# Optimization experiments

Measured on AMD Instinct MI355X. Metric: run time of the kernel, lower is better.

The kernel has to match this reference:

```python
import jax, jax.numpy as jnp
import numpy as np

EPS = 1e-6
CHUNK = 256
N_HEADS = 16
GATE_NORM = 16.0


def rmsnorm(x, eps=EPS):
    # RMSNorm without affine; normalizes over the last axis (matches custom
    # RMSNorm applied pre-view over full dim for q/k/v and over head_dim for subln)
    return x * jax.lax.rsqrt(jnp.mean(x * x, axis=-1, keepdims=True) + eps)


def chunk_gate_retention(q, k, v, gt, chunk_size):
    """Chunked gated linear attention (RetNet/GLA-style).
    Recurrence: S_t = exp(g_t) * S_{t-1} + k_t^T v_t;  o_t = q_t @ S_t.
    q,k,v: (b,h,t,d); gt: (b,h,t) log-decay. Returns (o, last_state)."""
    b, h, t, d = q.shape
    c = chunk_size
    n = t // c
    scale = d ** -0.5
    q = q.reshape(b, h, n, c, d) * scale
    k = k.reshape(b, h, n, c, d)
    v = v.reshape(b, h, n, c, d)
    g = gt.reshape(b, h, n, c)
    bc = jnp.cumsum(g, axis=-1)            # cumulative log-decay within chunk (incl. own gate)
    B = bc[..., -1:]                        # total chunk log-decay (b,h,n,1)
    # ---- intra-chunk (causal, decayed) ----
    decay = jnp.exp(bc[..., :, None] - bc[..., None, :])  # (b,h,n,c,c), <=1 on/below diag
    mask = jnp.tril(jnp.ones((c, c), dtype=bool))
    A = jnp.einsum('bhnid,bhnjd->bhnij', q, k) * jnp.where(mask, decay, 0.0)
    o_intra = jnp.einsum('bhnij,bhnjd->bhnid', A, v)
    # ---- per-chunk kv summaries (decay from position j to chunk end) ----
    kd = k * jnp.exp(B - bc)[..., None]
    kv = jnp.einsum('bhncd,bhnce->bhnde', kd, v)          # (b,h,n,d,d)
    qd = q * jnp.exp(bc)[..., None]                        # state decay into position i
    # ---- inter-chunk recurrence over chunk index ----
    def step(S, inp):
        qd_n, kv_n, B_n = inp
        o_cross = jnp.einsum('bhcd,bhde->bhce', qd_n, S)
        S_new = jnp.exp(B_n)[..., None] * S + kv_n
        return S_new, o_cross
    S0 = jnp.zeros((b, h, d, d), dtype=q.dtype)
    inps = (jnp.moveaxis(qd, 2, 0), jnp.moveaxis(kv, 2, 0), jnp.moveaxis(B, 2, 0))
    S_last, o_cross = jax.lax.scan(step, S0, inps)
    o_cross = jnp.moveaxis(o_cross, 0, 2)                  # (b,h,n,c,d)
    o = (o_intra + o_cross).reshape(b, h, t, d)
    return o, S_last


def setup_inputs() -> dict:
    key = jax.random.key(0)
    ks = jax.random.split(key, 7)
    dim, nh = 1024, N_HEADS
    s = 0.03  # keep activations sane
    return {
        'x':   jax.random.normal(ks[0], (2, 8192, dim), dtype=jnp.float32),
        'Wq':  jax.random.normal(ks[1], (dim, dim), dtype=jnp.float32) * s,
        'Wk':  jax.random.normal(ks[2], (dim, dim), dtype=jnp.float32) * s,
        'Wv':  jax.random.normal(ks[3], (dim, dim), dtype=jnp.float32) * s,
        'Wg':  jax.random.normal(ks[4], (dim, dim), dtype=jnp.float32) * s,
        'Wgt': jax.random.normal(ks[5], (dim, nh), dtype=jnp.float32) * s,
        'Wo':  jax.random.normal(ks[6], (dim, dim), dtype=jnp.float32) * s,
    }


def reference(x, Wq, Wk, Wv, Wg, Wgt, Wo):
    b, t, dim = x.shape
    h = N_HEADS
    d = dim // h
    q = rmsnorm(x @ Wq)
    k = rmsnorm(x @ Wk)
    v = rmsnorm(x @ Wv)
    g = x @ Wg
    gt = jax.nn.log_sigmoid(x @ Wgt) / GATE_NORM   # (b,t,h)
    qr = q.reshape(b, t, h, d).transpose(0, 2, 1, 3)
    kr = k.reshape(b, t, h, d).transpose(0, 2, 1, 3)
    vr = v.reshape(b, t, h, d).transpose(0, 2, 1, 3)
    gtr = gt.transpose(0, 2, 1)                    # (b,h,t)
    o, _ = chunk_gate_retention(qr, kr, vr, gtr, CHUNK)
    o = rmsnorm(o)                                 # subln over head_dim
    o = o.transpose(0, 2, 1, 3).reshape(b, t, dim)
    o = jax.nn.silu(g) * o                         # swiglu(g, o)
    return o @ Wo
```

## Files before the change

### kernel.cpp

```cpp
#include <hip/hip_runtime.h>

#define T_SEQ 8192
#define NH 16
#define HD 64
#define DIM 1024
#define ROWS 16384
#define CHK 256
#define NCHK 32

typedef float f32x4 __attribute__((ext_vector_type(4)));
typedef __bf16 bf16x8 __attribute__((ext_vector_type(8)));
typedef short short8 __attribute__((ext_vector_type(8)));
typedef short short4v __attribute__((ext_vector_type(4)));
typedef unsigned short ushort_t;

__device__ __forceinline__ float bf2f(ushort_t u){ return __uint_as_float(((unsigned)u)<<16); }
__device__ __forceinline__ ushort_t f2bf(float f){
  unsigned u = __float_as_uint(f);
  u += 0x7FFFu + ((u>>16)&1u);
  return (ushort_t)(u>>16);
}
#define BFLO(u) __uint_as_float((u)<<16)
#define BFHI(u) __uint_as_float((u)&0xFFFF0000u)
#define MFMA16(a,b,c) __builtin_amdgcn_mfma_f32_16x16x32_bf16((a),(b),(c),0,0,0)

__global__ __launch_bounds__(256) void transpose_all(const float* __restrict__ Wq,
    const float* __restrict__ Wk, const float* __restrict__ Wv,
    const float* __restrict__ Wg, const float* __restrict__ Wo,
    ushort_t* __restrict__ wcat, ushort_t* __restrict__ wot){
  int z = blockIdx.z;
  const float* W = (z==0)?Wq:(z==1)?Wk:(z==2)?Wv:(z==3)?Wg:Wo;
  ushort_t* D = (z<4)? (wcat + (size_t)z*DIM*DIM) : wot;
  __shared__ float tile[64][65];
  int k0 = blockIdx.x*64, n0 = blockIdx.y*64;
  int tid = threadIdx.x;
  #pragma unroll
  for (int it=0; it<16; ++it){
    int idx = tid + it*256;
    int r = idx>>6, c = idx&63;
    tile[r][c] = W[(size_t)(k0+r)*DIM + n0+c];
  }
  __syncthreads();
  #pragma unroll
  for (int it=0; it<16; ++it){
    int idx = tid + it*256;
    int r = idx>>6, c = idx&63;
    D[(size_t)(n0+r)*DIM + k0+c] = f2bf(tile[c][r]);
  }
}

template<int OUT_BF16>
__global__ __launch_bounds__(256,2) void gemm_bt(const ushort_t* __restrict__ A,
    const ushort_t* __restrict__ Bt, void* __restrict__ Cv, int M, int N, int K,
    float* __restrict__ ssqp){
  __shared__ __align__(16) ushort_t As[128*64];
  __shared__ __align__(16) ushort_t Bs[128*64];
  int tid = threadIdx.x;
  int lane = tid & 63, wid = tid >> 6;
  int wr = wid >> 1, wc = wid & 1;
  int m0 = blockIdx.x * 128, n0 = blockIdx.y * 128;
  f32x4 acc[4][4] = {};
  int srow = tid >> 3;
  int sg = tid & 7;
  const int nkt = K >> 6;
  for (int kt = 0; kt < nkt; ++kt){
    short8 ra[4], rb[4];
    #pragma unroll
    for (int s = 0; s < 4; ++s){
      int row = s*32 + srow;
      int gl = sg ^ (row & 7);
      ra[s] = *(const short8*)&A[(size_t)(m0 + row)*K + kt*64 + gl*8];
      rb[s] = *(const short8*)&Bt[(size_t)(n0 + row)*K + kt*64 + gl*8];
    }
    __syncthreads();
    #pragma unroll
    for (int s = 0; s < 4; ++s){
      int row = s*32 + srow;
      *(short8*)&As[row*64 + sg*8] = ra[s];
      *(short8*)&Bs[row*64 + sg*8] = rb[s];
    }
    __syncthreads();
    #pragma unroll
    for (int kk = 0; kk < 2; ++kk){
      bf16x8 af[4], bfv[4];
      #pragma unroll
      for (int m = 0; m < 4; ++m){
        int row = wr*64 + m*16 + (lane & 15);
        int g = kk*4 + (lane >> 4);
        af[m] = *(const bf16x8*)&As[row*64 + ((g ^ (row & 7))<<3)];
      }
      #pragma unroll
      for (int n = 0; n < 4; ++n){
        int row = wc*64 + n*16 + (lane & 15);
        int g = kk*4 + (lane >> 4);
        bfv[n] = *(const bf16x8*)&Bs[row*64 + ((g ^ (row & 7))<<3)];
      }
      #pragma unroll
      for (int m = 0; m < 4; ++m)
        #pragma unroll
        for (int n = 0; n < 4; ++n)
          acc[m][n] = MFMA16(af[m], bfv[n], acc[m][n]);
    }
  }
  #pragma unroll
  for (int m = 0; m < 4; ++m){
    int row = m0 + wr*64 + m*16 + (lane>>4)*4;
    #pragma unroll
    for (int n = 0; n < 4; ++n){
      int col = n0 + wc*64 + n*16 + (lane & 15);
      #pragma unroll
      for (int r = 0; r < 4; ++r){
        float v = acc[m][n][r];
        if (OUT_BF16) ((ushort_t*)Cv)[(size_t)(row+r)*N + col] = f2bf(v);
        else          ((float*)Cv)[(size_t)(row+r)*N + col] = v;
      }
    }
  }
  if (OUT_BF16 && blockIdx.y < 24){
    int slot = blockIdx.y*2 + wc;
    #pragma unroll
    for (int m = 0; m < 4; ++m){
      #pragma unroll
      for (int r = 0; r < 4; ++r){
        float s = 0.f;
        #pragma unroll
        for (int n = 0; n < 4; ++n){ float xx = acc[m][n][r]; s += xx*xx; }
        s += __shfl_xor(s,1); s += __shfl_xor(s,2);
        s += __shfl_xor(s,4); s += __shfl_xor(s,8);
        if ((lane & 15) == 0){
          int row = m0 + wr*64 + m*16 + (lane>>4)*4 + r;
          ssqp[(size_t)slot*ROWS + row] = s;
        }
      }
    }
  }
}

__global__ __launch_bounds__(256) void rms_combine(const float* __restrict__ ssqp,
                                                   float* __restrict__ rmsb){
  int idx = blockIdx.x*256 + threadIdx.x;
  int mat = idx >> 14, row = idx & (ROWS-1);
  float s = 0.f;
  #pragma unroll
  for (int k=0;k<16;++k) s += ssqp[(size_t)(mat*16+k)*ROWS + row];
  rmsb[idx] = rsqrtf(s*(1.f/1024.f)+1e-6f);
}

__global__ __launch_bounds__(256) void gt_ker(const float* __restrict__ x,
    const float* __restrict__ Wgt, float* __restrict__ gtb, ushort_t* __restrict__ xbf){
  int row = blockIdx.x; int b = row>>13; int t = row & (T_SEQ-1);
  int tid = threadIdx.x; int lane = tid&63; int w = tid>>6;
  __shared__ float xs[1024];
  #pragma unroll
  for (int i=0;i<4;++i) xs[tid+256*i] = x[(size_t)row*DIM + tid+256*i];
  __syncthreads();
  short4v xb4;
  #pragma unroll
  for (int k2=0;k2<4;++k2) xb4[k2] = (short)f2bf(xs[tid*4+k2]);
  *(short4v*)&xbf[(size_t)row*DIM + tid*4] = xb4;
  float a0=0,a1=0,a2=0,a3=0;
  #pragma unroll
  for (int jj=0;jj<16;++jj){
    int j = lane + 64*jj;
    float xv = xs[j];
    const float* wp = &Wgt[(size_t)j*NH + w*4];
    a0 += xv*wp[0]; a1 += xv*wp[1]; a2 += xv*wp[2]; a3 += xv*wp[3];
  }
  #pragma unroll
  for (int off=32; off>=1; off>>=1){
    a0 += __shfl_xor(a0, off); a1 += __shfl_xor(a1, off);
    a2 += __shfl_xor(a2, off); a3 += __shfl_xor(a3, off);
  }
  if (lane==0){
    float za[4] = {a0,a1,a2,a3};
    #pragma unroll
    for (int i=0;i<4;++i){
      float z = za[i];
      float ls = fminf(z,0.f) - log1pf(__expf(-fabsf(z)));
      gtb[((size_t)(b*NH + w*4 + i))*T_SEQ + t] = ls * (1.f/16.f);
    }
  }
}

__global__ __launch_bounds__(256,2) void attn_p1(const ushort_t* __restrict__ qkvg,
    const float* __restrict__ gtb, const float* __restrict__ rmsb,
    float* __restrict__ Bb, float* __restrict__ kvb){
  __shared__ __align__(16) ushort_t sh2[32768];
  ushort_t* kdt = sh2;
  ushort_t* vt  = sh2 + 16384;
  float* tmp = (float*)sh2;
  int bid = blockIdx.x; int n = bid&31; int bh = bid>>5; int b = bh>>4; int h = bh&15;
  int t0 = n*CHK; int tid = threadIdx.x; int lane = tid&63; int w = tid>>6;
  float vscan = gtb[(size_t)bh*T_SEQ + t0 + tid];
  #pragma unroll
  for (int off=1; off<64; off<<=1){ float u = __shfl_up(vscan, off); if (lane>=off) vscan += u; }
  if (lane==63) tmp[w] = vscan;
  __syncthreads();
  float pre=0;
  #pragma unroll
  for (int i=0;i<4;++i) if (i<w) pre += tmp[i];
  float bc = vscan + pre;
  float Bn = tmp[0]+tmp[1]+tmp[2]+tmp[3];
  if (tid==0) Bb[bid] = Bn;
  __syncthreads();
  {
    int j = tid;
    int grow = b*T_SEQ + t0 + j;
    size_t rowb = (size_t)grow*4096;
    float fk = rmsb[ROWS + grow] * __expf(Bn - bc);
    float fv = rmsb[2*ROWS + grow];
    #pragma unroll
    for (int q8=0; q8<8; ++q8){
      short8 k8 = *(const short8*)&qkvg[rowb + 1024 + h*HD + q8*8];
      short8 v8 = *(const short8*)&qkvg[rowb + 2048 + h*HD + q8*8];
      #pragma unroll
      for (int kk=0; kk<8; ++kk){
        int d = q8*8 + kk;
        kdt[(d<<8) + (((j>>3)^(d&7))<<3) + (j&7)] = f2bf(bf2f((ushort_t)k8[kk])*fk);
        vt [(d<<8) + (((j>>3)^(d&7))<<3) + (j&7)] = f2bf(bf2f((ushort_t)v8[kk])*fv);
      }
    }
  }
  __syncthreads();
  f32x4 acc[4] = {};
  #pragma unroll
  for (int s=0; s<8; ++s){
    int d = w*16 + (lane&15);
    int jj = s*32 + (lane>>4)*8;
    bf16x8 ka = *(const bf16x8*)&kdt[(d<<8) + (((jj>>3)^(d&7))<<3)];
    #pragma unroll
    for (int et=0; et<4; ++et){
      int e = et*16 + (lane&15);
      bf16x8 vf = *(const bf16x8*)&vt[(e<<8) + (((jj>>3)^(e&7))<<3)];
      acc[et] = MFMA16(ka, vf, acc[et]);
    }
  }
  float* kvp = &kvb[(size_t)bid*4096];
  #pragma unroll
  for (int et=0; et<4; ++et)
    #pragma unroll
    for (int r=0; r<4; ++r)
      kvp[(et*16 + (lane&15))*64 + w*16 + (lane>>4)*4 + r] = acc[et][r];
}

__global__ __launch_bounds__(256) void scan_ker(const float* __restrict__ kvb,
    const float* __restrict__ Bb, ushort_t* __restrict__ Sb){
  int gidx = blockIdx.x*256 + threadIdx.x;
  int bh = gidx >> 12; int f = gidx & 4095;
  float S = 0.f;
  const float* kp = &kvb[(size_t)bh*NCHK*4096 + f];
  ushort_t* sp = &Sb[(size_t)bh*NCHK*4096 + f];
  for (int n=0;n<NCHK;++n){
    sp[(size_t)n*4096] = f2bf(S);
    S = __expf(Bb[bh*NCHK+n])*S + kp[(size_t)n*4096];
  }
}

__global__ __launch_bounds__(512,2) void attn_p3(const ushort_t* __restrict__ qkvg,
    const float* __restrict__ gtb, const float* __restrict__ rmsb,
    const ushort_t* __restrict__ Sb, ushort_t* __restrict__ oact){
  __shared__ __align__(16) ushort_t sh[(32768+16384+1024+32+2048)/2];
  ushort_t* vt = sh;
  ushort_t* ps = sh + 16384;
  float* bcs = (float*)(sh + 24576);
  float* tmp = (float*)(sh + 25088);
  float* rqs = (float*)(sh + 25104);
  float* rks = (float*)(sh + 25616);
  int bid = blockIdx.x; int n = bid&31; int bh = bid>>5; int b = bh>>4; int h = bh&15;
  int t0 = n*CHK; int tid = threadIdx.x; int lane = tid&63; int w = tid>>6;
  float vscan = 0.f;
  if (tid < 256){
    vscan = gtb[(size_t)bh*T_SEQ + t0 + tid];
    #pragma unroll
    for (int off=1; off<64; off<<=1){ float u = __shfl_up(vscan, off); if (lane>=off) vscan += u; }
    if (lane==63) tmp[w] = vscan;
  }
  __syncthreads();
  if (tid < 256){
    float pre=0;
    #pragma unroll
    for (int i=0;i<4;++i) if (i<w) pre += tmp[i];
    bcs[tid] = vscan + pre;
    int grow = b*T_SEQ + t0 + tid;
    rqs[tid] = rmsb[grow];
    rks[tid] = rmsb[ROWS + grow];
  }
  {
    int j = tid>>1, ehalf = tid&1;
    int grow = b*T_SEQ + t0 + j;
    size_t rowb = (size_t)grow*4096;
    float fv = rmsb[2*ROWS + grow];
    #pragma unroll
    for (int q8=0; q8<4; ++q8){
      short8 v8 = *(const short8*)&qkvg[rowb + 2048 + h*HD + ehalf*32 + q8*8];
      #pragma unroll
      for (int kk=0; kk<8; ++kk){
        int e = ehalf*32 + q8*8 + kk;
        vt[(e<<8) + (((j>>3)^(e&7))<<3) + (j&7)] = f2bf(bf2f((ushort_t)v8[kk])*fv);
      }
    }
  }
  __syncthreads();
  int wrow = w*32;
  size_t chunkbase = (size_t)b*T_SEQ + t0;
  bf16x8 qf[2][2];
  #pragma unroll
  for (int rt=0; rt<2; ++rt)
    #pragma unroll
    for (int s=0; s<2; ++s)
      qf[rt][s] = *(const bf16x8*)&qkvg[(chunkbase + wrow + rt*16 + (lane&15))*4096
                                        + h*HD + s*32 + (lane>>4)*8];
  f32x4 o_[2][4] = {};
  #pragma unroll
  for (int s=0; s<2; ++s)
    #pragma unroll
    for (int et=0; et<4; ++et){
      bf16x8 stf = *(const bf16x8*)&Sb[(size_t)bid*4096 + (et*16 + (lane&15))*64
                                       + s*32 + (lane>>4)*8];
      #pragma unroll
      for (int rt=0; rt<2; ++rt)
        o_[rt][et] = MFMA16(qf[rt][s], stf, o_[rt][et]);
    }
  #pragma unroll
  for (int rt=0; rt<2; ++rt)
    #pragma unroll
    for (int rr=0; rr<4; ++rr){
      int ri = wrow + rt*16 + (lane>>4)*4 + rr;
      float fs = 0.125f*__expf(bcs[ri])*rqs[ri];
      #pragma unroll
      for (int et=0; et<4; ++et) o_[rt][et][rr] *= fs;
    }
  for (int hb=0; hb<=w; ++hb){
    int jb = hb>>1, ch = hb&1;
    int jbase = jb*64 + ch*32;
    float mb = bcs[jb*64];
    float r8[2][4];
    #pragma unroll
    for (int rt=0; rt<2; ++rt)
      #pragma unroll
      for (int rr=0; rr<4; ++rr){
        int ri = wrow + rt*16 + (lane>>4)*4 + rr;
        r8[rt][rr] = 0.125f*__expf(bcs[ri] - mb)*rqs[ri];
      }
    float c2[2];
    #pragma unroll
    for (int ct=0; ct<2; ++ct){
      int jc = jbase + ct*16 + (lane&15);
      c2[ct] = __expf(mb - bcs[jc])*rks[jc];
    }
    f32x4 s2[2][2] = {};
    #pragma unroll
    for (int s=0; s<2; ++s)
      #pragma unroll
      for (int ct=0; ct<2; ++ct){
        bf16x8 kf = *(const bf16x8*)&qkvg[(chunkbase + jbase + ct*16 + (lane&15))*4096
                                          + 1024 + h*HD + s*32 + (lane>>4)*8];
        #pragma unroll
        for (int rt=0; rt<2; ++rt)
          s2[rt][ct] = MFMA16(qf[rt][s], kf, s2[rt][ct]);
      }
    bool dia = (hb == w);
    #pragma unroll
    for (int rt=0; rt<2; ++rt)
      #pragma unroll
      for (int ct=0; ct<2; ++ct)
        #pragma unroll
        for (int rr=0; rr<4; ++rr){
          int pi = rt*16 + (lane>>4)*4 + rr;
          int pj = ct*16 + (lane&15);
          float pv = s2[rt][ct][rr] * r8[rt][rr] * c2[ct];
          if (dia && (jbase + pj) > (wrow + pi)) pv = 0.f;
          ps[w*1024 + pi*32 + (((pj>>3) ^ ((pi>>2)&3))<<3) + (pj&7)] = f2bf(pv);
        }
    bf16x8 vf[4];
    #pragma unroll
    for (int et=0; et<4; ++et){
      int e = et*16 + (lane&15);
      int jj = jbase + (lane>>4)*8;
      vf[et] = *(const bf16x8*)&vt[(e<<8) + (((jj>>3) ^ (e&7))<<3)];
    }
    bf16x8 pf[2];
    #pragma unroll
    for (int rt=0; rt<2; ++rt){
      int i = rt*16 + (lane&15);
      pf[rt] = *(const bf16x8*)&ps[w*1024 + i*32 + (((lane>>4) ^ ((i>>2)&3))<<3)];
    }
    #pragma unroll
    for (int rt=0; rt<2; ++rt)
      #pragma unroll
      for (int et=0; et<4; ++et)
        o_[rt][et] = MFMA16(pf[rt], vf[et], o_[rt][et]);
  }
  float rms8[2][4];
  #pragma unroll
  for (int rt=0; rt<2; ++rt)
    #pragma unroll
    for (int rr=0; rr<4; ++rr){
      float ssq = 0.f;
      #pragma unroll
      for (int et=0; et<4; ++et){ float xx = o_[rt][et][rr]; ssq += xx*xx; }
      ssq += __shfl_xor(ssq,1); ssq += __shfl_xor(ssq,2);
      ssq += __shfl_xor(ssq,4); ssq += __shfl_xor(ssq,8);
      rms8[rt][rr] = rsqrtf(ssq*(1.f/64.f)+1e-6f);
    }
  #pragma unroll
  for (int eh=0; eh<2; ++eh){
    #pragma unroll
    for (int rt=0; rt<2; ++rt)
      #pragma unroll
      for (int e2=0; e2<2; ++e2){
        int et = eh*2 + e2;
        #pragma unroll
        for (int rr=0; rr<4; ++rr){
          int pi = rt*16 + (lane>>4)*4 + rr;
          int pj = e2*16 + (lane&15);
          ps[w*1024 + pi*32 + (((pj>>3) ^ ((pi>>2)&3))<<3) + (pj&7)] =
            f2bf(o_[rt][et][rr]*rms8[rt][rr]);
        }
      }
    int i2 = lane&31, e16 = (lane>>5)*16;
    int gr0 = e16>>3;
    int f = (i2>>2)&3;
    short8 ov0 = *(const short8*)&ps[w*1024 + i2*32 + ((gr0^f)<<3)];
    short8 ov1 = *(const short8*)&ps[w*1024 + i2*32 + (((gr0+1)^f)<<3)];
    size_t rowg = chunkbase + wrow + i2;
    short8 gv0 = *(const short8*)&qkvg[rowg*4096 + 3072 + h*HD + eh*32 + e16];
    short8 gv1 = *(const short8*)&qkvg[rowg*4096 + 3072 + h*HD + eh*32 + e16 + 8];
    ushort_t outv[16];
    #pragma unroll
    for (int k=0;k<8;++k){
      float gf = bf2f((ushort_t)gv0[k]);
      float sg = gf/(1.f+__expf(-gf));
      outv[k] = f2bf(bf2f((ushort_t)ov0[k])*sg);
    }
    #pragma unroll
    for (int k=0;k<8;++k){
      float gf = bf2f((ushort_t)gv1[k]);
      float sg = gf/(1.f+__expf(-gf));
      outv[8+k] = f2bf(bf2f((ushort_t)ov1[k])*sg);
    }
    ushort_t* op = &oact[rowg*DIM + h*HD + eh*32 + e16];
    *(short8*)&op[0] = *(short8*)&outv[0];
    *(short8*)&op[8] = *(short8*)&outv[8];
  }
}

extern "C" void kernel_launch(void* const* d_in, const int* in_sizes, int n_in,
                              void* d_out, int out_size, void* d_ws, size_t ws_size,
                              hipStream_t stream){
  const float* x  = (const float*)d_in[0];
  const float* Wq = (const float*)d_in[1];
  const float* Wk = (const float*)d_in[2];
  const float* Wv = (const float*)d_in[3];
  const float* Wg = (const float*)d_in[4];
  const float* Wgt= (const float*)d_in[5];
  const float* Wo = (const float*)d_in[6];
  float* out = (float*)d_out;

  char* p = (char*)d_ws;
  ushort_t* xbf  = (ushort_t*)p; p += (size_t)ROWS*DIM*2;
  ushort_t* wcat = (ushort_t*)p; p += (size_t)4*DIM*DIM*2;
  ushort_t* wot  = (ushort_t*)p; p += (size_t)DIM*DIM*2;
  ushort_t* qkvg = (ushort_t*)p; p += (size_t)ROWS*4096*2;
  float* gtb = (float*)p; p += (size_t)32*T_SEQ*4;
  float* Bb  = (float*)p; p += 1024*4;
  float* kvb = (float*)p; p += (size_t)1024*4096*4;
  ushort_t* Sb = (ushort_t*)p; p += (size_t)1024*4096*2;
  ushort_t* oact = (ushort_t*)p; p += (size_t)ROWS*DIM*2;
  float* ssqp = (float*)p; p += (size_t)48*ROWS*4;
  float* rmsb = (float*)p; p += (size_t)3*ROWS*4;
  if ((size_t)(p - (char*)d_ws) > ws_size) return;

  gt_ker<<<ROWS,256,0,stream>>>(x, Wgt, gtb, xbf);
  transpose_all<<<dim3(16,16,5),256,0,stream>>>(Wq, Wk, Wv, Wg, Wo, wcat, wot);
  gemm_bt<1><<<dim3(ROWS/128, 4096/128), 256, 0, stream>>>(xbf, wcat, qkvg, ROWS, 4096, DIM, ssqp);
  rms_combine<<<(3*ROWS)/256,256,0,stream>>>(ssqp, rmsb);
  attn_p1<<<1024,256,0,stream>>>(qkvg, gtb, rmsb, Bb, kvb);
  scan_ker<<<512,256,0,stream>>>(kvb, Bb, Sb);
  attn_p3<<<1024,512,0,stream>>>(qkvg, gtb, rmsb, Sb, oact);
  gemm_bt<0><<<dim3(ROWS/128, 1024/128), 256, 0, stream>>>(oact, wot, out, ROWS, 1024, DIM, nullptr);
}
```

Before: 393.6 us.

## Balance causal work across waves in attn_p3 and widen attn_p1 loading

In attn_p3 each wave now owns two 16-row tiles taken from opposite ends of the chunk (w and 15-w) instead of 32 contiguous rows, so every wave handles a similar number of causal key blocks. The old triangular imbalance between waves is removed, and inactive tiles skip their MFMAs through act0 guards. attn_p1 now launches 512 threads so twice as many threads load and scale K/V into LDS, while only four waves run the MFMA accumulation. The cost is extra branching and idle waves during attn_p1's compute phase.

```diff
diff --git a/kernel.cpp b/kernel.cpp
--- a/kernel.cpp
+++ b/kernel.cpp
@@ -182,65 +182,73 @@
   }
 }
 
-__global__ __launch_bounds__(256,2) void attn_p1(const ushort_t* __restrict__ qkvg,
+__global__ __launch_bounds__(512,2) void attn_p1(const ushort_t* __restrict__ qkvg,
     const float* __restrict__ gtb, const float* __restrict__ rmsb,
     float* __restrict__ Bb, float* __restrict__ kvb){
   __shared__ __align__(16) ushort_t sh2[32768];
+  __shared__ float bcf[256];
+  __shared__ float tmp4[4];
   ushort_t* kdt = sh2;
   ushort_t* vt  = sh2 + 16384;
-  float* tmp = (float*)sh2;
   int bid = blockIdx.x; int n = bid&31; int bh = bid>>5; int b = bh>>4; int h = bh&15;
   int t0 = n*CHK; int tid = threadIdx.x; int lane = tid&63; int w = tid>>6;
-  float vscan = gtb[(size_t)bh*T_SEQ + t0 + tid];
-  #pragma unroll
-  for (int off=1; off<64; off<<=1){ float u = __shfl_up(vscan, off); if (lane>=off) vscan += u; }
-  if (lane==63) tmp[w] = vscan;
-  __syncthreads();
-  float pre=0;
-  #pragma unroll
-  for (int i=0;i<4;++i) if (i<w) pre += tmp[i];
-  float bc = vscan + pre;
-  float Bn = tmp[0]+tmp[1]+tmp[2]+tmp[3];
+  float vscan = 0.f;
+  if (tid < 256){
+    vscan = gtb[(size_t)bh*T_SEQ + t0 + tid];
+    #pragma unroll
+    for (int off=1; off<64; off<<=1){ float u = __shfl_up(vscan, off); if (lane>=off) vscan += u; }
+    if (lane==63) tmp4[w] = vscan;
+  }
+  __syncthreads();
+  float Bn = tmp4[0]+tmp4[1]+tmp4[2]+tmp4[3];
+  if (tid < 256){
+    float pre=0;
+    #pragma unroll
+    for (int i=0;i<4;++i) if (i<w) pre += tmp4[i];
+    bcf[tid] = vscan + pre;
+  }
   if (tid==0) Bb[bid] = Bn;
   __syncthreads();
   {
-    int j = tid;
+    int j = tid>>1, dh = tid&1;
     int grow = b*T_SEQ + t0 + j;
     size_t rowb = (size_t)grow*4096;
-    float fk = rmsb[ROWS + grow] * __expf(Bn - bc);
+    float fk = rmsb[ROWS + grow] * __expf(Bn - bcf[j]);
     float fv = rmsb[2*ROWS + grow];
     #pragma unroll
-    for (int q8=0; q8<8; ++q8){
-      short8 k8 = *(const short8*)&qkvg[rowb + 1024 + h*HD + q8*8];
-      short8 v8 = *(const short8*)&qkvg[rowb + 2048 + h*HD + q8*8];
+    for (int q8=0; q8<4; ++q8){
+      short8 k8 = *(const short8*)&qkvg[rowb + 1024 + h*HD + dh*32 + q8*8];
+      short8 v8 = *(const short8*)&qkvg[rowb + 2048 + h*HD + dh*32 + q8*8];
       #pragma unroll
       for (int kk=0; kk<8; ++kk){
-        int d = q8*8 + kk;
+        int d = dh*32 + q8*8 + kk;
         kdt[(d<<8) + (((j>>3)^(d&7))<<3) + (j&7)] = f2bf(bf2f((ushort_t)k8[kk])*fk);
         vt [(d<<8) + (((j>>3)^(d&7))<<3) + (j&7)] = f2bf(bf2f((ushort_t)v8[kk])*fv);
       }
     }
   }
   __syncthreads();
-  f32x4 acc[4] = {};
-  #pragma unroll
-  for (int s=0; s<8; ++s){
-    int d = w*16 + (lane&15);
-    int jj = s*32 + (lane>>4)*8;
-    bf16x8 ka = *(const bf16x8*)&kdt[(d<<8) + (((jj>>3)^(d&7))<<3)];
-    #pragma unroll
-    for (int et=0; et<4; ++et){
-      int e = et*16 + (lane&15);
-      bf16x8 vf = *(const bf16x8*)&vt[(e<<8) + (((jj>>3)^(e&7))<<3)];
-      acc[et] = MFMA16(ka, vf, acc[et]);
-    }
-  }
-  float* kvp = &kvb[(size_t)bid*4096];
-  #pragma unroll
-  for (int et=0; et<4; ++et)
-    #pragma unroll
-    for (int r=0; r<4; ++r)
-      kvp[(et*16 + (lane&15))*64 + w*16 + (lane>>4)*4 + r] = acc[et][r];
+  if (w < 4){
+    f32x4 acc[4] = {};
+    #pragma unroll
+    for (int s=0; s<8; ++s){
+      int d = w*16 + (lane&15);
+      int jj = s*32 + (lane>>4)*8;
+      bf16x8 ka = *(const bf16x8*)&kdt[(d<<8) + (((jj>>3)^(d&7))<<3)];
+      #pragma unroll
+      for (int et=0; et<4; ++et){
+        int e = et*16 + (lane&15);
+        bf16x8 vf = *(const bf16x8*)&vt[(e<<8) + (((jj>>3)^(e&7))<<3)];
+        acc[et] = MFMA16(ka, vf, acc[et]);
+      }
+    }
+    float* kvp = &kvb[(size_t)bid*4096];
+    #pragma unroll
+    for (int et=0; et<4; ++et)
+      #pragma unroll
+      for (int r=0; r<4; ++r)
+        kvp[(et*16 + (lane&15))*64 + w*16 + (lane>>4)*4 + r] = acc[et][r];
+  }
 }
 
 __global__ __launch_bounds__(256) void scan_ker(const float* __restrict__ kvb,
@@ -301,15 +309,16 @@
     }
   }
   __syncthreads();
-  int wrow = w*32;
+  int rb0 = w*16, rb1 = (15-w)*16;
   size_t chunkbase = (size_t)b*T_SEQ + t0;
   bf16x8 qf[2][2];
   #pragma unroll
-  for (int rt=0; rt<2; ++rt)
-    #pragma unroll
-    for (int s=0; s<2; ++s)
-      qf[rt][s] = *(const bf16x8*)&qkvg[(chunkbase + wrow + rt*16 + (lane&15))*4096
-                                        + h*HD + s*32 + (lane>>4)*8];
+  for (int s=0; s<2; ++s){
+    qf[0][s] = *(const bf16x8*)&qkvg[(chunkbase + rb0 + (lane&15))*4096
+                                      + h*HD + s*32 + (lane>>4)*8];
+    qf[1][s] = *(const bf16x8*)&qkvg[(chunkbase + rb1 + (lane&15))*4096
+                                      + h*HD + s*32 + (lane>>4)*8];
+  }
   f32x4 o_[2][4] = {};
   #pragma unroll
   for (int s=0; s<2; ++s)
@@ -317,31 +326,34 @@
     for (int et=0; et<4; ++et){
       bf16x8 stf = *(const bf16x8*)&Sb[(size_t)bid*4096 + (et*16 + (lane&15))*64
                                        + s*32 + (lane>>4)*8];
-      #pragma unroll
-      for (int rt=0; rt<2; ++rt)
-        o_[rt][et] = MFMA16(qf[rt][s], stf, o_[rt][et]);
+      o_[0][et] = MFMA16(qf[0][s], stf, o_[0][et]);
+      o_[1][et] = MFMA16(qf[1][s], stf, o_[1][et]);
     }
   #pragma unroll
   for (int rt=0; rt<2; ++rt)
     #pragma unroll
     for (int rr=0; rr<4; ++rr){
-      int ri = wrow + rt*16 + (lane>>4)*4 + rr;
+      int ri = (rt? rb1 : rb0) + (lane>>4)*4 + rr;
       float fs = 0.125f*__expf(bcs[ri])*rqs[ri];
       #pragma unroll
       for (int et=0; et<4; ++et) o_[rt][et][rr] *= fs;
     }
-  for (int hb=0; hb<=w; ++hb){
-    int jb = hb>>1, ch = hb&1;
-    int jbase = jb*64 + ch*32;
-    float mb = bcs[jb*64];
+  int h0max = w >> 1;
+  int hbmax = (15 - w) >> 1;
+  for (int hb=0; hb<=hbmax; ++hb){
+    int jbase = hb*32;
+    float mb = bcs[(hb>>1)*64];
+    bool act0 = (hb <= h0max);
+    bool dia0 = (hb == h0max);
+    bool dia1 = (hb == hbmax);
     float r8[2][4];
     #pragma unroll
-    for (int rt=0; rt<2; ++rt)
-      #pragma unroll
-      for (int rr=0; rr<4; ++rr){
-        int ri = wrow + rt*16 + (lane>>4)*4 + rr;
-        r8[rt][rr] = 0.125f*__expf(bcs[ri] - mb)*rqs[ri];
-      }
+    for (int rr=0; rr<4; ++rr){
+      int ri0 = rb0 + (lane>>4)*4 + rr;
+      int ri1 = rb1 + (lane>>4)*4 + rr;
+      r8[0][rr] = act0 ? 0.125f*__expf(bcs[ri0] - mb)*rqs[ri0] : 0.f;
+      r8[1][rr] = 0.125f*__expf(bcs[ri1] - mb)*rqs[ri1];
+    }
     float c2[2];
     #pragma unroll
     for (int ct=0; ct<2; ++ct){
@@ -355,23 +367,32 @@
       for (int ct=0; ct<2; ++ct){
         bf16x8 kf = *(const bf16x8*)&qkvg[(chunkbase + jbase + ct*16 + (lane&15))*4096
                                           + 1024 + h*HD + s*32 + (lane>>4)*8];
-        #pragma unroll
-        for (int rt=0; rt<2; ++rt)
-          s2[rt][ct] = MFMA16(qf[rt][s], kf, s2[rt][ct]);
-      }
-    bool dia = (hb == w);
-    #pragma unroll
-    for (int rt=0; rt<2; ++rt)
+        s2[1][ct] = MFMA16(qf[1][s], kf, s2[1][ct]);
+        if (act0) s2[0][ct] = MFMA16(qf[0][s], kf, s2[0][ct]);
+      }
+    #pragma unroll
+    for (int ct=0; ct<2; ++ct)
+      #pragma unroll
+      for (int rr=0; rr<4; ++rr){
+        int pil = (lane>>4)*4 + rr;
+        int pj = ct*16 + (lane&15);
+        float pv = s2[1][ct][rr] * r8[1][rr] * c2[ct];
+        if (dia1 && (jbase + pj) > (rb1 + pil)) pv = 0.f;
+        int pi = 16 + pil;
+        ps[w*1024 + pi*32 + (((pj>>3) ^ ((pi>>2)&3))<<3) + (pj&7)] = f2bf(pv);
+      }
+    if (act0){
       #pragma unroll
       for (int ct=0; ct<2; ++ct)
         #pragma unroll
         for (int rr=0; rr<4; ++rr){
-          int pi = rt*16 + (lane>>4)*4 + rr;
+          int pil = (lane>>4)*4 + rr;
           int pj = ct*16 + (lane&15);
-          float pv = s2[rt][ct][rr] * r8[rt][rr] * c2[ct];
-          if (dia && (jbase + pj) > (wrow + pi)) pv = 0.f;
-          ps[w*1024 + pi*32 + (((pj>>3) ^ ((pi>>2)&3))<<3) + (pj&7)] = f2bf(pv);
+          float pv = s2[0][ct][rr] * r8[0][rr] * c2[ct];
+          if (dia0 && (jbase + pj) > (rb0 + pil)) pv = 0.f;
+          ps[w*1024 + pil*32 + (((pj>>3) ^ ((pil>>2)&3))<<3) + (pj&7)] = f2bf(pv);
         }
+    }
     bf16x8 vf[4];
     #pragma unroll
     for (int et=0; et<4; ++et){
@@ -379,17 +400,20 @@
       int jj = jbase + (lane>>4)*8;
       vf[et] = *(const bf16x8*)&vt[(e<<8) + (((jj>>3) ^ (e&7))<<3)];
     }
-    bf16x8 pf[2];
-    #pragma unroll
-    for (int rt=0; rt<2; ++rt){
-      int i = rt*16 + (lane&15);
-      pf[rt] = *(const bf16x8*)&ps[w*1024 + i*32 + (((lane>>4) ^ ((i>>2)&3))<<3)];
-    }
-    #pragma unroll
-    for (int rt=0; rt<2; ++rt)
+    {
+      int i1 = 16 + (lane&15);
+      bf16x8 pf1 = *(const bf16x8*)&ps[w*1024 + i1*32 + (((lane>>4) ^ ((i1>>2)&3))<<3)];
       #pragma unroll
       for (int et=0; et<4; ++et)
-        o_[rt][et] = MFMA16(pf[rt], vf[et], o_[rt][et]);
+        o_[1][et] = MFMA16(pf1, vf[et], o_[1][et]);
+    }
+    if (act0){
+      int i0 = lane&15;
+      bf16x8 pf0 = *(const bf16x8*)&ps[w*1024 + i0*32 + (((lane>>4) ^ ((i0>>2)&3))<<3)];
+      #pragma unroll
+      for (int et=0; et<4; ++et)
+        o_[0][et] = MFMA16(pf0, vf[et], o_[0][et]);
+    }
   }
   float rms8[2][4];
   #pragma unroll
@@ -423,7 +447,8 @@
     int f = (i2>>2)&3;
     short8 ov0 = *(const short8*)&ps[w*1024 + i2*32 + ((gr0^f)<<3)];
     short8 ov1 = *(const short8*)&ps[w*1024 + i2*32 + (((gr0+1)^f)<<3)];
-    size_t rowg = chunkbase + wrow + i2;
+    int rowin = (i2 < 16) ? (rb0 + i2) : (rb1 + (i2&15));
+    size_t rowg = chunkbase + rowin;
     short8 gv0 = *(const short8*)&qkvg[rowg*4096 + 3072 + h*HD + eh*32 + e16];
     short8 gv1 = *(const short8*)&qkvg[rowg*4096 + 3072 + h*HD + eh*32 + e16 + 8];
     ushort_t outv[16];
@@ -475,7 +500,7 @@
   transpose_all<<<dim3(16,16,5),256,0,stream>>>(Wq, Wk, Wv, Wg, Wo, wcat, wot);
   gemm_bt<1><<<dim3(ROWS/128, 4096/128), 256, 0, stream>>>(xbf, wcat, qkvg, ROWS, 4096, DIM, ssqp);
   rms_combine<<<(3*ROWS)/256,256,0,stream>>>(ssqp, rmsb);
-  attn_p1<<<1024,256,0,stream>>>(qkvg, gtb, rmsb, Bb, kvb);
+  attn_p1<<<1024,512,0,stream>>>(qkvg, gtb, rmsb, Bb, kvb);
   scan_ker<<<512,256,0,stream>>>(kvb, Bb, Sb);
   attn_p3<<<1024,512,0,stream>>>(qkvg, gtb, rmsb, Sb, oact);
   gemm_bt<0><<<dim3(ROWS/128, 1024/128), 256, 0, stream>>>(oact, wot, out, ROWS, 1024, DIM, nullptr);
```

After: 408.3 us. 1.04x slower.
